# Kernel optimization log

Hardware: AMD Instinct MI355X
Metric: run time of the kernel (lower is better)

The kernel has to match this reference:

```python
import jax, jax.numpy as jnp
import numpy as np

NUM_HEADS = 16
HEAD_DIM = 64
HIDDEN = NUM_HEADS * HEAD_DIM  # 1024
Q_DIM = 512
KV_DIM = 256


def setup_inputs() -> dict:
    key = jax.random.key(0)
    k1, k2, k3, k4, k5, k6 = jax.random.split(key, 6)
    B, I, J = 64, 128, 512  # num_assets, num_latents, window_size
    q = jax.random.normal(k1, (B, I, Q_DIM), dtype=jnp.float32)
    kv = jax.random.normal(k2, (B, J, KV_DIM), dtype=jnp.float32)
    # Linear weights stored as (in, out); fan-in scaled init
    Wq = jax.random.normal(k3, (Q_DIM, HIDDEN), dtype=jnp.float32) / np.sqrt(Q_DIM)
    Wkv = jax.random.normal(k4, (KV_DIM, 2 * HIDDEN), dtype=jnp.float32) / np.sqrt(KV_DIM)
    Wo = jax.random.normal(k5, (HIDDEN, Q_DIM), dtype=jnp.float32) / np.sqrt(HIDDEN)
    bo = jax.random.normal(k6, (Q_DIM,), dtype=jnp.float32) * 0.01
    return {"q": q, "kv": kv, "Wq": Wq, "Wkv": Wkv, "Wo": Wo, "bo": bo}


def reference(q, kv, Wq, Wkv, Wo, bo):
    B, I, _ = q.shape
    J = kv.shape[1]
    scale = HEAD_DIM ** -0.5
    query = q @ Wq                              # (B, I, HIDDEN)
    k, v = jnp.split(kv @ Wkv, 2, axis=-1)      # each (B, J, HIDDEN)
    qh = query.reshape(B, I, NUM_HEADS, HEAD_DIM).transpose(0, 2, 1, 3)  # bhid
    kh = k.reshape(B, J, NUM_HEADS, HEAD_DIM).transpose(0, 2, 1, 3)      # bhjd
    vh = v.reshape(B, J, NUM_HEADS, HEAD_DIM).transpose(0, 2, 1, 3)      # bhjd
    scores = jnp.einsum('bhid,bhjd->bhij', qh, kh) * scale
    attn = jax.nn.softmax(scores, axis=-1)
    out = jnp.einsum('bhij,bhjd->bhid', attn, vh)
    out = out.transpose(0, 2, 1, 3).reshape(B, I, HIDDEN)
    return out @ Wo + bo
```

## Files before the change

kernel.cpp:

```cpp
#include <hip/hip_runtime.h>
#include <stdint.h>

typedef unsigned short ushort_t;
typedef __attribute__((ext_vector_type(8))) short short8;
typedef __attribute__((ext_vector_type(4))) float floatx4;
typedef __attribute__((ext_vector_type(4))) float floatv4;
typedef __attribute__((ext_vector_type(4))) unsigned short ushortv4;


__device__ __forceinline__ ushort_t f2bf(float x) {
    union { float f; unsigned u; } v; v.f = x;
    unsigned r = v.u + 0x7fffu + ((v.u >> 16) & 1u);
    return (ushort_t)(r >> 16);
}

__device__ __forceinline__ void gl_lds16(const ushort_t* g, ushort_t* l) {
    __builtin_amdgcn_global_load_lds(
        (const __attribute__((address_space(1))) void*)g,
        (__attribute__((address_space(3))) void*)l, 16, 0, 0);
}

__global__ __launch_bounds__(256) void prep_kernel(
    const float* __restrict__ q, const float* __restrict__ kv,
    const float* __restrict__ Wq, const float* __restrict__ Wkv,
    const float* __restrict__ Wo,
    ushort_t* __restrict__ qA, ushort_t* __restrict__ kvA,
    ushort_t* __restrict__ WqT, ushort_t* __restrict__ WkvT,
    ushort_t* __restrict__ WoT)
{
    __shared__ ushort_t tileS[64 * 68];
    const int bid = blockIdx.x;
    const int tid = threadIdx.x;
    if (bid < 4096) {
        int t = bid * 256 + tid;
        floatv4 v = ((const floatv4*)q)[t];
        ushortv4 o;
        o[0] = f2bf(v[0]); o[1] = f2bf(v[1]); o[2] = f2bf(v[2]); o[3] = f2bf(v[3]);
        ((ushortv4*)qA)[t] = o;
        return;
    }
    if (bid < 12288) {
        int t = (bid - 4096) * 256 + tid;
        floatv4 v = ((const floatv4*)kv)[t];
        ushortv4 o;
        o[0] = f2bf(v[0]); o[1] = f2bf(v[1]); o[2] = f2bf(v[2]); o[3] = f2bf(v[3]);
        ((ushortv4*)kvA)[t] = o;
        return;
    }
    const float* src; ushort_t* dst; int K, N, kt, nt; float scale = 1.0f;
    if (bid < 12416)      { int tl = bid - 12288; src = Wq;  dst = WqT;  K = 512;  N = 1024; kt = tl >> 4; nt = tl & 15; scale = 0.125f; }
    else if (bid < 12544) { int tl = bid - 12416; src = Wkv; dst = WkvT; K = 256;  N = 2048; kt = tl >> 5; nt = tl & 31; }
    else                  { int tl = bid - 12544; src = Wo;  dst = WoT;  K = 1024; N = 512;  kt = tl >> 3; nt = tl & 7;  }
#pragma unroll
    for (int t = 0; t < 4; t++) {
        int e = t * 256 + tid;
        int row = e >> 4, c4 = e & 15;
        floatv4 v = *(const floatv4*)&src[(size_t)(kt * 64 + row) * N + nt * 64 + c4 * 4];
        ushortv4 o;
        o[0] = f2bf(v[0] * scale); o[1] = f2bf(v[1] * scale);
        o[2] = f2bf(v[2] * scale); o[3] = f2bf(v[3] * scale);
        *(ushortv4*)&tileS[row * 68 + c4 * 4] = o;
    }
    __syncthreads();
#pragma unroll
    for (int t = 0; t < 4; t++) {
        int e = t * 256 + tid;
        int orow = e >> 4, c4 = e & 15;
        ushortv4 o;
#pragma unroll
        for (int e2 = 0; e2 < 4; e2++) o[e2] = tileS[(c4 * 4 + e2) * 68 + orow];
        *(ushortv4*)&dst[(size_t)(nt * 64 + orow) * K + kt * 64 + c4 * 4] = o;
    }
}

__global__ __launch_bounds__(256, 3) void gemm_bt_kernel(
    const ushort_t* __restrict__ A, const ushort_t* __restrict__ Bt,
    int M, int N, int K, int gx, int gy, int emode,
    ushort_t* __restrict__ out_a,
    float* __restrict__ out_f, const float* __restrict__ bias)
{
    __shared__ ushort_t smem[16896];
    ushort_t* sA = smem;
    ushort_t* sB = smem + 8192;
    ushort_t* sT = smem;

    const int bid  = blockIdx.x;
    const int xcd  = bid & 7;
    const int slot = bid >> 3;
    const int band = gy >> 3;
    const int by   = xcd * band + slot % band;
    const int bx   = slot / band;

    const int tid  = threadIdx.x;
    const int lane = tid & 63;
    const int w    = tid >> 6;
    const int quad = lane >> 4;
    const int l15  = lane & 15;
    const int wr   = w >> 1, wc = w & 1;
    const int m0 = by * 128;
    const int n0 = bx * 128;

    const int rsub = lane >> 3;
    const int c8   = lane & 7;
    const int wrow = w * 32;

    floatx4 acc[4][4];
#pragma unroll
    for (int i = 0; i < 4; i++)
#pragma unroll
        for (int j = 0; j < 4; j++) acc[i][j] = (floatx4){0.f, 0.f, 0.f, 0.f};

    for (int k0 = 0; k0 < K; k0 += 64) {
        __syncthreads();
#pragma unroll
        for (int t = 0; t < 4; t++) {
            int rg = wrow + t * 8;
            gl_lds16(&A[(size_t)(m0 + rg + rsub) * K + k0 + c8 * 8], &sA[rg * 64]);
            gl_lds16(&Bt[(size_t)(n0 + rg + rsub) * K + k0 + c8 * 8], &sB[rg * 64]);
        }
        __syncthreads();
#pragma unroll
        for (int ks = 0; ks < 64; ks += 32) {
            short8 af[4], bf[4];
#pragma unroll
            for (int i = 0; i < 4; i++)
                af[i] = *(const short8*)&sA[(wr * 64 + i * 16 + l15) * 64 + ks + quad * 8];
#pragma unroll
            for (int j = 0; j < 4; j++)
                bf[j] = *(const short8*)&sB[(wc * 64 + j * 16 + l15) * 64 + ks + quad * 8];
#pragma unroll
            for (int i = 0; i < 4; i++)
#pragma unroll
                for (int j = 0; j < 4; j++)
                    acc[i][j] = __builtin_amdgcn_mfma_f32_16x16x32_bf16(
                        af[i], bf[j], acc[i][j], 0, 0, 0);
        }
    }

    if (emode == 2) {
#pragma unroll
        for (int i = 0; i < 4; i++)
#pragma unroll
            for (int j = 0; j < 4; j++)
#pragma unroll
                for (int r = 0; r < 4; r++) {
                    int grow = m0 + wr * 64 + i * 16 + quad * 4 + r;
                    int gcol = n0 + wc * 64 + j * 16 + l15;
                    out_f[(size_t)grow * N + gcol] = acc[i][j][r] + bias[gcol];
                }
        return;
    }

    __syncthreads();
#pragma unroll
    for (int i = 0; i < 4; i++)
#pragma unroll
        for (int j = 0; j < 4; j++)
#pragma unroll
            for (int r = 0; r < 4; r++) {
                int row = wr * 64 + i * 16 + quad * 4 + r;
                int col = wc * 64 + j * 16 + l15;
                sT[row * 132 + col] = f2bf(acc[i][j][r]);
            }
    __syncthreads();
#pragma unroll
    for (int it = 0; it < 8; it++) {
        int idx = it * 256 + tid;
        int row = idx >> 4, chunk = idx & 15;
        short8 v = *(const short8*)&sT[row * 132 + chunk * 8];
        *(short8*)&out_a[(size_t)(m0 + row) * 1024 + n0 + chunk * 8] = v;
    }
}

__global__ __launch_bounds__(512, 4) void fattn_kernel(
    const ushort_t* __restrict__ QA,
    const ushort_t* __restrict__ WQ,
    const ushort_t* __restrict__ KV,
    const ushort_t* __restrict__ W,
    ushort_t* __restrict__ O)
{
    __shared__ ushort_t smem[35328];
    ushort_t* sKV = smem;
    ushort_t* sKc = smem + 16896;
    ushort_t* sVt = smem + 21504;
    ushort_t* sP  = smem + 26112;
    ushort_t* sQ  = smem;
    ushort_t* sW  = smem + 17408;

    const int bid  = blockIdx.x;
    const int xcd  = bid & 7;
    const int slot = bid >> 3;
    const int b = xcd * 8 + (slot & 7);
    const int h = slot >> 3;

    const int tid  = threadIdx.x;
    const int lane = tid & 63, w = tid >> 6;
    const int quad = lane >> 4, l15 = lane & 15;

    ushort_t* sp = &sP[w * 1152];

    const ushort_t* qb = &QA[(size_t)b * 128 * 512];
    const ushort_t* wq = &WQ[(size_t)h * 64 * 512];
    floatx4 qacc[4];
#pragma unroll
    for (int nt = 0; nt < 4; nt++) qacc[nt] = (floatx4){0.f, 0.f, 0.f, 0.f};

    for (int kc = 0; kc < 4; kc++) {
        if (kc) __syncthreads();
#pragma unroll
        for (int t = 0; t < 4; t++) {
            int c = tid + t * 512;
            int row = c >> 4, cc = c & 15;
            *(short8*)&sQ[row * 136 + cc * 8] =
                *(const short8*)&qb[(size_t)row * 512 + kc * 128 + cc * 8];
        }
#pragma unroll
        for (int t = 0; t < 2; t++) {
            int c = tid + t * 512;
            int row = c >> 4, cc = c & 15;
            *(short8*)&sW[row * 136 + cc * 8] =
                *(const short8*)&wq[(size_t)row * 512 + kc * 128 + cc * 8];
        }
        __syncthreads();
#pragma unroll
        for (int ks = 0; ks < 4; ks++) {
            short8 af = *(const short8*)&sQ[(w * 16 + l15) * 136 + ks * 32 + quad * 8];
#pragma unroll
            for (int nt = 0; nt < 4; nt++) {
                short8 bfr = *(const short8*)&sW[(nt * 16 + l15) * 136 + ks * 32 + quad * 8];
                qacc[nt] = __builtin_amdgcn_mfma_f32_16x16x32_bf16(af, bfr, qacc[nt], 0, 0, 0);
            }
        }
    }
    __syncthreads();

#pragma unroll
    for (int nt = 0; nt < 4; nt++)
#pragma unroll
        for (int r = 0; r < 4; r++)
            sp[(quad * 4 + r) * 72 + nt * 16 + l15] = f2bf(qacc[nt][r]);
    short8 aq0 = *(const short8*)&sp[l15 * 72 + quad * 8];
    short8 aq1 = *(const short8*)&sp[l15 * 72 + 32 + quad * 8];

    short8 wf[8];
    {
        int n = w * 16 + l15;
        int grow = (n < 64) ? (h * 64 + n) : (1024 + h * 64 + (n - 64));
        const ushort_t* wp = &W[(size_t)grow * 256 + quad * 8];
#pragma unroll
        for (int ks = 0; ks < 8; ks++)
            wf[ks] = *(const short8*)(wp + ks * 32);
    }

    float lsum[4];
    floatx4 acc_o[4];
#pragma unroll
    for (int r = 0; r < 4; r++) lsum[r] = 0.f;
#pragma unroll
    for (int dt = 0; dt < 4; dt++) acc_o[dt] = (floatx4){0.f, 0.f, 0.f, 0.f};

    for (int ch = 0; ch < 8; ch++) {
        const int j0 = ch * 64;
#pragma unroll
        for (int t = 0; t < 4; t++) {
            int c = tid + t * 512;
            int row = c >> 5, cc = c & 31;
            *(short8*)&sKV[row * 264 + cc * 8] =
                *(const short8*)&KV[(size_t)(b * 512 + j0 + row) * 256 + cc * 8];
        }
        __syncthreads();

        floatx4 pacc[4];
#pragma unroll
        for (int jt = 0; jt < 4; jt++) pacc[jt] = (floatx4){0.f, 0.f, 0.f, 0.f};
#pragma unroll
        for (int ks = 0; ks < 8; ks++) {
            short8 af[4];
#pragma unroll
            for (int jt = 0; jt < 4; jt++)
                af[jt] = *(const short8*)&sKV[(jt * 16 + l15) * 264 + ks * 32 + quad * 8];
#pragma unroll
            for (int jt = 0; jt < 4; jt++)
                pacc[jt] = __builtin_amdgcn_mfma_f32_16x16x32_bf16(
                    af[jt], wf[ks], pacc[jt], 0, 0, 0);
        }

        if (w < 4) {
            int d = w * 16 + l15;
#pragma unroll
            for (int jt = 0; jt < 4; jt++)
#pragma unroll
                for (int r = 0; r < 4; r++)
                    sKc[(jt * 16 + quad * 4 + r) * 72 + d] = f2bf(pacc[jt][r]);
        } else {
            int d = (w - 4) * 16 + l15;
#pragma unroll
            for (int jt = 0; jt < 4; jt++) {
                ushortv4 p;
#pragma unroll
                for (int r = 0; r < 4; r++) p[r] = f2bf(pacc[jt][r]);
                *(ushortv4*)&sVt[d * 72 + jt * 16 + quad * 4] = p;
            }
        }
        __syncthreads();

#pragma unroll
        for (int jt = 0; jt < 4; jt++) {
            const ushort_t* kp = &sKc[(jt * 16 + l15) * 72 + quad * 8];
            short8 bk0 = *(const short8*)kp;
            short8 bk1 = *(const short8*)(kp + 32);
            floatx4 a = (floatx4){0.f, 0.f, 0.f, 0.f};
            a = __builtin_amdgcn_mfma_f32_16x16x32_bf16(aq0, bk0, a, 0, 0, 0);
            a = __builtin_amdgcn_mfma_f32_16x16x32_bf16(aq1, bk1, a, 0, 0, 0);
            ushortv4 pk;
#pragma unroll
            for (int r = 0; r < 4; r++) {
                float p = __expf(a[r]);
                lsum[r] += p;
                pk[r] = f2bf(p);
            }
#pragma unroll
            for (int r = 0; r < 4; r++)
                sp[(quad * 4 + r) * 72 + jt * 16 + l15] = pk[r];
        }

#pragma unroll
        for (int kk = 0; kk < 2; kk++) {
            short8 ap = *(const short8*)&sp[l15 * 72 + kk * 32 + quad * 8];
#pragma unroll
            for (int dt = 0; dt < 4; dt++) {
                short8 bv = *(const short8*)&sVt[(dt * 16 + l15) * 72 + kk * 32 + quad * 8];
                acc_o[dt] = __builtin_amdgcn_mfma_f32_16x16x32_bf16(ap, bv, acc_o[dt], 0, 0, 0);
            }
        }
    }

#pragma unroll
    for (int r = 0; r < 4; r++) {
        float s = lsum[r];
#pragma unroll
        for (int off = 1; off < 16; off <<= 1) s += __shfl_xor(s, off);
        float inv = 1.0f / s;
        size_t rowo = (size_t)(b * 128 + w * 16 + quad * 4 + r) * 1024 + h * 64;
#pragma unroll
        for (int dt = 0; dt < 4; dt++)
            O[rowo + dt * 16 + l15] = f2bf(acc_o[dt][r] * inv);
    }
}

extern "C" void kernel_launch(void* const* d_in, const int* in_sizes, int n_in,
                              void* d_out, int out_size, void* d_ws, size_t ws_size,
                              hipStream_t stream) {
    const float* q   = (const float*)d_in[0];
    const float* kv  = (const float*)d_in[1];
    const float* Wq  = (const float*)d_in[2];
    const float* Wkv = (const float*)d_in[3];
    const float* Wo  = (const float*)d_in[4];
    const float* bo  = (const float*)d_in[5];
    float* out = (float*)d_out;

    char* ws = (char*)d_ws;
    ushort_t* qA    = (ushort_t*)(ws + 0);
    ushort_t* kvA   = (ushort_t*)(ws + 8388608);
    ushort_t* WqT   = (ushort_t*)(ws + 25165824);
    ushort_t* WkvT  = (ushort_t*)(ws + 26214400);
    ushort_t* WoT   = (ushort_t*)(ws + 27262976);
    ushort_t* attnO = (ushort_t*)(ws + 45088768);

    hipLaunchKernelGGL(prep_kernel, dim3(12672), dim3(256), 0, stream,
                       q, kv, Wq, Wkv, Wo, qA, kvA, WqT, WkvT, WoT);

    hipLaunchKernelGGL(fattn_kernel, dim3(1024), dim3(512), 0, stream,
                       qA, WqT, kvA, WkvT, attnO);

    hipLaunchKernelGGL(gemm_bt_kernel, dim3(256), dim3(256), 0, stream,
                       attnO, WoT, 8192, 512, 1024, 4, 64, 2, (ushort_t*)nullptr,
                       out, bo);
}
```

Before: 213.4 us.

## Pre-swizzle q, kv and Wq into MFMA fragment order, drop LDS staging in attention

```diff
diff --git a/kernel.cpp b/kernel.cpp
--- a/kernel.cpp
+++ b/kernel.cpp
@@ -24,42 +24,98 @@
     const float* __restrict__ q, const float* __restrict__ kv,
     const float* __restrict__ Wq, const float* __restrict__ Wkv,
     const float* __restrict__ Wo,
-    ushort_t* __restrict__ qA, ushort_t* __restrict__ kvA,
-    ushort_t* __restrict__ WqT, ushort_t* __restrict__ WkvT,
+    ushort_t* __restrict__ qS, ushort_t* __restrict__ kvS,
+    ushort_t* __restrict__ WqS, ushort_t* __restrict__ WkvT,
     ushort_t* __restrict__ WoT)
 {
-    __shared__ ushort_t tileS[64 * 68];
+    __shared__ ushort_t sT[16896];
     const int bid = blockIdx.x;
     const int tid = threadIdx.x;
-    if (bid < 4096) {
-        int t = bid * 256 + tid;
-        floatv4 v = ((const floatv4*)q)[t];
-        ushortv4 o;
-        o[0] = f2bf(v[0]); o[1] = f2bf(v[1]); o[2] = f2bf(v[2]); o[3] = f2bf(v[3]);
-        ((ushortv4*)qA)[t] = o;
+
+    if (bid < 512) {
+        const int b = bid >> 3, jg = bid & 7;
+        const float* src = &kv[(size_t)(b * 512 + jg * 64) * 256];
+#pragma unroll
+        for (int it = 0; it < 16; it++) {
+            int idx = it * 256 + tid;
+            int row = idx >> 6, c4 = idx & 63;
+            floatv4 v = *(const floatv4*)&src[(size_t)row * 256 + c4 * 4];
+            ushortv4 o;
+            o[0] = f2bf(v[0]); o[1] = f2bf(v[1]); o[2] = f2bf(v[2]); o[3] = f2bf(v[3]);
+            *(ushortv4*)&sT[row * 264 + c4 * 4] = o;
+        }
+        __syncthreads();
+        ushort_t* dst = &kvS[(size_t)(b * 32 + jg * 4) * 8 * 512];
+#pragma unroll
+        for (int it = 0; it < 8; it++) {
+            int c = it * 256 + tid;
+            int fblk = c >> 6, lane = c & 63;
+            int jt = fblk >> 3, ks = fblk & 7;
+            int mm = lane & 15, qd = lane >> 4;
+            short8 vv = *(const short8*)&sT[(jt * 16 + mm) * 264 + ks * 32 + qd * 8];
+            *(short8*)&dst[(size_t)fblk * 512 + lane * 8] = vv;
+        }
         return;
     }
-    if (bid < 12288) {
-        int t = (bid - 4096) * 256 + tid;
-        floatv4 v = ((const floatv4*)kv)[t];
-        ushortv4 o;
-        o[0] = f2bf(v[0]); o[1] = f2bf(v[1]); o[2] = f2bf(v[2]); o[3] = f2bf(v[3]);
-        ((ushortv4*)kvA)[t] = o;
+    if (bid < 768) {
+        const int blk = bid - 512, b = blk >> 2, ig = blk & 3;
+        const float* src = &q[(size_t)(b * 128 + ig * 32) * 512];
+#pragma unroll
+        for (int it = 0; it < 16; it++) {
+            int idx = it * 256 + tid;
+            int row = idx >> 7, c4 = idx & 127;
+            floatv4 v = *(const floatv4*)&src[(size_t)row * 512 + c4 * 4];
+            ushortv4 o;
+            o[0] = f2bf(v[0]); o[1] = f2bf(v[1]); o[2] = f2bf(v[2]); o[3] = f2bf(v[3]);
+            *(ushortv4*)&sT[row * 520 + c4 * 4] = o;
+        }
+        __syncthreads();
+        ushort_t* dst = &qS[(size_t)(b * 8 + ig * 2) * 16 * 512];
+#pragma unroll
+        for (int it = 0; it < 8; it++) {
+            int c = it * 256 + tid;
+            int fblk = c >> 6, lane = c & 63;
+            int it2 = fblk >> 4, ks = fblk & 15;
+            int mm = lane & 15, qd = lane >> 4;
+            short8 vv = *(const short8*)&sT[(it2 * 16 + mm) * 520 + ks * 32 + qd * 8];
+            *(short8*)&dst[(size_t)fblk * 512 + lane * 8] = vv;
+        }
         return;
     }
-    const float* src; ushort_t* dst; int K, N, kt, nt; float scale = 1.0f;
-    if (bid < 12416)      { int tl = bid - 12288; src = Wq;  dst = WqT;  K = 512;  N = 1024; kt = tl >> 4; nt = tl & 15; scale = 0.125f; }
-    else if (bid < 12544) { int tl = bid - 12416; src = Wkv; dst = WkvT; K = 256;  N = 2048; kt = tl >> 5; nt = tl & 31; }
-    else                  { int tl = bid - 12544; src = Wo;  dst = WoT;  K = 1024; N = 512;  kt = tl >> 3; nt = tl & 7;  }
+    if (bid < 800) {
+        const int blk = bid - 768, h = blk >> 1, kh = blk & 1;
+#pragma unroll
+        for (int it = 0; it < 16; it++) {
+            int idx = it * 256 + tid;
+            int row = idx >> 4, c4 = idx & 15;
+            floatv4 v = *(const floatv4*)&Wq[(size_t)(kh * 256 + row) * 1024 + h * 64 + c4 * 4];
+#pragma unroll
+            for (int e = 0; e < 4; e++)
+                sT[(c4 * 4 + e) * 264 + row] = f2bf(v[e] * 0.125f);
+        }
+        __syncthreads();
+#pragma unroll
+        for (int it = 0; it < 8; it++) {
+            int c = it * 256 + tid;
+            int fblk = c >> 6, lane = c & 63;
+            int nt = fblk >> 3, ksl = fblk & 7;
+            int mm = lane & 15, qd = lane >> 4;
+            short8 vv = *(const short8*)&sT[(nt * 16 + mm) * 264 + ksl * 32 + qd * 8];
+            *(short8*)&WqS[((size_t)(h * 4 + nt) * 16 + kh * 8 + ksl) * 512 + lane * 8] = vv;
+        }
+        return;
+    }
+    const float* src; ushort_t* dst; int K, N, kt, nt;
+    if (bid < 928) { int tl = bid - 800; src = Wkv; dst = WkvT; K = 256;  N = 2048; kt = tl >> 5; nt = tl & 31; }
+    else           { int tl = bid - 928; src = Wo;  dst = WoT;  K = 1024; N = 512;  kt = tl >> 3; nt = tl & 7;  }
 #pragma unroll
     for (int t = 0; t < 4; t++) {
         int e = t * 256 + tid;
         int row = e >> 4, c4 = e & 15;
         floatv4 v = *(const floatv4*)&src[(size_t)(kt * 64 + row) * N + nt * 64 + c4 * 4];
         ushortv4 o;
-        o[0] = f2bf(v[0] * scale); o[1] = f2bf(v[1] * scale);
-        o[2] = f2bf(v[2] * scale); o[3] = f2bf(v[3] * scale);
-        *(ushortv4*)&tileS[row * 68 + c4 * 4] = o;
+        o[0] = f2bf(v[0]); o[1] = f2bf(v[1]); o[2] = f2bf(v[2]); o[3] = f2bf(v[3]);
+        *(ushortv4*)&sT[row * 68 + c4 * 4] = o;
     }
     __syncthreads();
 #pragma unroll
@@ -68,7 +124,7 @@
         int orow = e >> 4, c4 = e & 15;
         ushortv4 o;
 #pragma unroll
-        for (int e2 = 0; e2 < 4; e2++) o[e2] = tileS[(c4 * 4 + e2) * 68 + orow];
+        for (int e2 = 0; e2 < 4; e2++) o[e2] = sT[(c4 * 4 + e2) * 68 + orow];
         *(ushortv4*)&dst[(size_t)(nt * 64 + orow) * K + kt * 64 + c4 * 4] = o;
     }
 }
@@ -82,7 +138,6 @@
     __shared__ ushort_t smem[16896];
     ushort_t* sA = smem;
     ushort_t* sB = smem + 8192;
-    ushort_t* sT = smem;
 
     const int bid  = blockIdx.x;
     const int xcd  = bid & 7;
@@ -137,55 +192,28 @@
         }
     }
 
-    if (emode == 2) {
-#pragma unroll
-        for (int i = 0; i < 4; i++)
-#pragma unroll
-            for (int j = 0; j < 4; j++)
-#pragma unroll
-                for (int r = 0; r < 4; r++) {
-                    int grow = m0 + wr * 64 + i * 16 + quad * 4 + r;
-                    int gcol = n0 + wc * 64 + j * 16 + l15;
-                    out_f[(size_t)grow * N + gcol] = acc[i][j][r] + bias[gcol];
-                }
-        return;
-    }
-
-    __syncthreads();
 #pragma unroll
     for (int i = 0; i < 4; i++)
 #pragma unroll
         for (int j = 0; j < 4; j++)
 #pragma unroll
             for (int r = 0; r < 4; r++) {
-                int row = wr * 64 + i * 16 + quad * 4 + r;
-                int col = wc * 64 + j * 16 + l15;
-                sT[row * 132 + col] = f2bf(acc[i][j][r]);
+                int grow = m0 + wr * 64 + i * 16 + quad * 4 + r;
+                int gcol = n0 + wc * 64 + j * 16 + l15;
+                out_f[(size_t)grow * N + gcol] = acc[i][j][r] + bias[gcol];
             }
-    __syncthreads();
-#pragma unroll
-    for (int it = 0; it < 8; it++) {
-        int idx = it * 256 + tid;
-        int row = idx >> 4, chunk = idx & 15;
-        short8 v = *(const short8*)&sT[row * 132 + chunk * 8];
-        *(short8*)&out_a[(size_t)(m0 + row) * 1024 + n0 + chunk * 8] = v;
-    }
 }
 
 __global__ __launch_bounds__(512, 4) void fattn_kernel(
-    const ushort_t* __restrict__ QA,
-    const ushort_t* __restrict__ WQ,
-    const ushort_t* __restrict__ KV,
+    const ushort_t* __restrict__ qS,
+    const ushort_t* __restrict__ WqS,
+    const ushort_t* __restrict__ kvS,
     const ushort_t* __restrict__ W,
     ushort_t* __restrict__ O)
 {
-    __shared__ ushort_t smem[35328];
-    ushort_t* sKV = smem;
-    ushort_t* sKc = smem + 16896;
-    ushort_t* sVt = smem + 21504;
-    ushort_t* sP  = smem + 26112;
-    ushort_t* sQ  = smem;
-    ushort_t* sW  = smem + 17408;
+    __shared__ ushort_t sKc[64 * 72];
+    __shared__ ushort_t sVt[64 * 72];
+    __shared__ ushort_t sP[8 * 16 * 72];
 
     const int bid  = blockIdx.x;
     const int xcd  = bid & 7;
@@ -199,41 +227,20 @@
 
     ushort_t* sp = &sP[w * 1152];
 
-    const ushort_t* qb = &QA[(size_t)b * 128 * 512];
-    const ushort_t* wq = &WQ[(size_t)h * 64 * 512];
+    const ushort_t* qf  = &qS[((size_t)(b * 8 + w) * 16) * 512 + lane * 8];
+    const ushort_t* wqf = &WqS[((size_t)h * 64) * 512 + lane * 8];
     floatx4 qacc[4];
 #pragma unroll
     for (int nt = 0; nt < 4; nt++) qacc[nt] = (floatx4){0.f, 0.f, 0.f, 0.f};
-
-    for (int kc = 0; kc < 4; kc++) {
-        if (kc) __syncthreads();
-#pragma unroll
-        for (int t = 0; t < 4; t++) {
-            int c = tid + t * 512;
-            int row = c >> 4, cc = c & 15;
-            *(short8*)&sQ[row * 136 + cc * 8] =
-                *(const short8*)&qb[(size_t)row * 512 + kc * 128 + cc * 8];
-        }
-#pragma unroll
-        for (int t = 0; t < 2; t++) {
-            int c = tid + t * 512;
-            int row = c >> 4, cc = c & 15;
-            *(short8*)&sW[row * 136 + cc * 8] =
-                *(const short8*)&wq[(size_t)row * 512 + kc * 128 + cc * 8];
-        }
-        __syncthreads();
-#pragma unroll
-        for (int ks = 0; ks < 4; ks++) {
-            short8 af = *(const short8*)&sQ[(w * 16 + l15) * 136 + ks * 32 + quad * 8];
-#pragma unroll
-            for (int nt = 0; nt < 4; nt++) {
-                short8 bfr = *(const short8*)&sW[(nt * 16 + l15) * 136 + ks * 32 + quad * 8];
-                qacc[nt] = __builtin_amdgcn_mfma_f32_16x16x32_bf16(af, bfr, qacc[nt], 0, 0, 0);
-            }
-        }
-    }
-    __syncthreads();
-
+#pragma unroll
+    for (int ks = 0; ks < 16; ks++) {
+        short8 af = *(const short8*)(qf + (size_t)ks * 512);
+#pragma unroll
+        for (int nt = 0; nt < 4; nt++) {
+            short8 bfr = *(const short8*)(wqf + (size_t)(nt * 16 + ks) * 512);
+            qacc[nt] = __builtin_amdgcn_mfma_f32_16x16x32_bf16(af, bfr, qacc[nt], 0, 0, 0);
+        }
+    }
 #pragma unroll
     for (int nt = 0; nt < 4; nt++)
 #pragma unroll
@@ -260,16 +267,7 @@
     for (int dt = 0; dt < 4; dt++) acc_o[dt] = (floatx4){0.f, 0.f, 0.f, 0.f};
 
     for (int ch = 0; ch < 8; ch++) {
-        const int j0 = ch * 64;
-#pragma unroll
-        for (int t = 0; t < 4; t++) {
-            int c = tid + t * 512;
-            int row = c >> 5, cc = c & 31;
-            *(short8*)&sKV[row * 264 + cc * 8] =
-                *(const short8*)&KV[(size_t)(b * 512 + j0 + row) * 256 + cc * 8];
-        }
-        __syncthreads();
-
+        const ushort_t* kvf = &kvS[((size_t)(b * 32 + ch * 4) * 8) * 512 + lane * 8];
         floatx4 pacc[4];
 #pragma unroll
         for (int jt = 0; jt < 4; jt++) pacc[jt] = (floatx4){0.f, 0.f, 0.f, 0.f};
@@ -278,12 +276,14 @@
             short8 af[4];
 #pragma unroll
             for (int jt = 0; jt < 4; jt++)
-                af[jt] = *(const short8*)&sKV[(jt * 16 + l15) * 264 + ks * 32 + quad * 8];
+                af[jt] = *(const short8*)(kvf + (size_t)(jt * 8 + ks) * 512);
 #pragma unroll
             for (int jt = 0; jt < 4; jt++)
                 pacc[jt] = __builtin_amdgcn_mfma_f32_16x16x32_bf16(
                     af[jt], wf[ks], pacc[jt], 0, 0, 0);
         }
+
+        __syncthreads();
 
         if (w < 4) {
             int d = w * 16 + l15;
@@ -360,18 +360,18 @@
     float* out = (float*)d_out;
 
     char* ws = (char*)d_ws;
-    ushort_t* qA    = (ushort_t*)(ws + 0);
-    ushort_t* kvA   = (ushort_t*)(ws + 8388608);
-    ushort_t* WqT   = (ushort_t*)(ws + 25165824);
+    ushort_t* kvS   = (ushort_t*)(ws + 0);
+    ushort_t* qS    = (ushort_t*)(ws + 16777216);
+    ushort_t* WqS   = (ushort_t*)(ws + 25165824);
     ushort_t* WkvT  = (ushort_t*)(ws + 26214400);
     ushort_t* WoT   = (ushort_t*)(ws + 27262976);
-    ushort_t* attnO = (ushort_t*)(ws + 45088768);
-
-    hipLaunchKernelGGL(prep_kernel, dim3(12672), dim3(256), 0, stream,
-                       q, kv, Wq, Wkv, Wo, qA, kvA, WqT, WkvT, WoT);
+    ushort_t* attnO = (ushort_t*)(ws + 28311552);
+
+    hipLaunchKernelGGL(prep_kernel, dim3(1056), dim3(256), 0, stream,
+                       q, kv, Wq, Wkv, Wo, qS, kvS, WqS, WkvT, WoT);
 
     hipLaunchKernelGGL(fattn_kernel, dim3(1024), dim3(512), 0, stream,
-                       qA, WqT, kvA, WkvT, attnO);
+                       qS, WqS, kvS, WkvT, attnO);
 
     hipLaunchKernelGGL(gemm_bt_kernel, dim3(256), dim3(256), 0, stream,
                        attnO, WoT, 8192, 512, 1024, 4, 64, 2, (ushort_t*)nullptr,
```

Result: slower. 221.5 us (+3.8%).
